# Kernel optimization log

Measured on AMD Instinct MI355X. Metric: run time of the kernel, lower is better.

Reference implementation:

```python
import jax, jax.numpy as jnp
import numpy as np

B, I, O, G = 4096, 256, 256, 8
GRID_MIN, GRID_MAX, RHO = -2.0, 2.0, 1.0


def setup_inputs() -> dict:
    key = jax.random.key(0)
    ks = jax.random.split(key, 8)
    return {
        "x_re": jax.random.normal(ks[0], (B, I), dtype=jnp.float32),
        "x_im": jax.random.normal(ks[1], (B, I), dtype=jnp.float32),
        "realweights": jax.random.normal(ks[2], (I, O, G, G), dtype=jnp.float32),
        "complexweights": jax.random.normal(ks[3], (I, O, G, G), dtype=jnp.float32),
        "silu_weight_re": jax.random.normal(ks[4], (I, O), dtype=jnp.float32),
        "silu_weight_im": jax.random.normal(ks[5], (I, O), dtype=jnp.float32),
        "silu_bias_re": 0.1 * jax.random.normal(ks[6], (I, O), dtype=jnp.float32),
        "silu_bias_im": 0.1 * jax.random.normal(ks[7], (I, O), dtype=jnp.float32),
    }


def reference(x_re, x_im, realweights, complexweights,
              silu_weight_re, silu_weight_im, silu_bias_re, silu_bias_im):
    # Complex grid: grid[u, v] = lin[u] + i * lin[v]
    lin = jnp.linspace(GRID_MIN, GRID_MAX, G, dtype=x_re.dtype)
    # |x - grid|^2 = (x_re - lin_u)^2 + (x_im - lin_v)^2  -> (B, I, G, G)
    dre = x_re[:, :, None, None] - lin[None, None, :, None]
    dim = x_im[:, :, None, None] - lin[None, None, None, :]
    basis = jnp.exp(-(dre * dre + dim * dim) / RHO)  # real-valued (B, I, G, G)
    # RBF contraction: real and imaginary output channels
    out_re = jnp.einsum('biuv,iouv->bo', basis, realweights)
    out_im = jnp.einsum('biuv,iouv->bo', basis, complexweights)
    # Complex SiLU (complex_weight variant): silu applied component-wise,
    # then complex-multiplied by silu_weight, plus bias, summed over i.
    s_re = jax.nn.silu(x_re)  # (B, I)
    s_im = jax.nn.silu(x_im)
    out_re = out_re + s_re @ silu_weight_re - s_im @ silu_weight_im + jnp.sum(silu_bias_re, axis=0)
    out_im = out_im + s_im @ silu_weight_re + s_re @ silu_weight_im + jnp.sum(silu_bias_im, axis=0)
    # Return complex output as stacked (real, imag): (B, O, 2)
    return jnp.stack([out_re, out_im], axis=-1)
```

## Files before the change

kernel.cpp:

```cpp
#include <hip/hip_runtime.h>
#include <hip/hip_fp16.h>
#include <stdint.h>

typedef float floatx4 __attribute__((ext_vector_type(4)));
typedef short short8 __attribute__((ext_vector_type(8)));

constexpr int I_SZ = 256, O_SZ = 256, NCOL = 512, B_SZ = 4096;
constexpr int KSTEPS = 264;
constexpr float GSTEP = 4.0f / 7.0f;
constexpr float NLOG2E = -1.44269504088896f;

__device__ __forceinline__ uint32_t pk_bf16(float lo, float hi) {
  return __builtin_amdgcn_perm(__float_as_uint(hi), __float_as_uint(lo), 0x07060302u);
}
__device__ __forceinline__ short rne_bf16(float f) {
  uint32_t u = __float_as_uint(f);
  return (short)((u + 0x7FFFu + ((u >> 16) & 1u)) >> 16);
}
__device__ __forceinline__ float silu_f(float a) {
  return a * __builtin_amdgcn_rcpf(1.f + __builtin_amdgcn_exp2f(a * NLOG2E));
}
__device__ __forceinline__ void gload_lds16(const void* g, void* l) {
  __builtin_amdgcn_global_load_lds((const __attribute__((address_space(1))) void*)g,
                                   (__attribute__((address_space(3))) void*)l,
                                   16, 0, 0);
}

__global__ void prelude(const float* __restrict__ rw, const float* __restrict__ cw,
                        const float* __restrict__ swre, const float* __restrict__ swim,
                        const float* __restrict__ bre, const float* __restrict__ bim,
                        const float* __restrict__ xre, const float* __restrict__ xim,
                        short* __restrict__ wpack, float* __restrict__ bsum,
                        __half* __restrict__ xT, float* __restrict__ out) {
  __shared__ float tile[64][65];
  const int bid = blockIdx.x, tid = threadIdx.x;

  if (bid < 4224) {
    int idx = bid * 256 + tid;
    int kb = idx >> 12;
    int rem = idx & 4095;
    int n = rem >> 3, gp = rem & 7;
    int g = gp ^ (n & 7);
    int o = n >> 1, c = n & 1;
    float w[8];
    if (kb < 256) {
      const float* W = (c ? cw : rw) + (((size_t)kb * O_SZ + o) << 6) + (g << 3);
      float4 a = *(const float4*)W;
      float4 b = *(const float4*)(W + 4);
      w[0] = a.x; w[1] = a.y; w[2] = a.z; w[3] = a.w;
      w[4] = b.x; w[5] = b.y; w[6] = b.z; w[7] = b.w;
    } else {
      int kp0 = ((kb - 256) << 6) + (g << 3);
      #pragma unroll
      for (int e = 0; e < 8; ++e) {
        int kp = kp0 + e, i = kp >> 1, ci = kp & 1;
        float a = swre[i * O_SZ + o], b = swim[i * O_SZ + o];
        w[e] = (c == 0) ? (ci == 0 ? a : -b) : (ci == 0 ? b : a);
      }
    }
    uint32_t h[8];
    #pragma unroll
    for (int e = 0; e < 8; ++e) h[e] = (uint32_t)(uint16_t)rne_bf16(w[e]);
    uint4 val = make_uint4(h[0] | (h[1] << 16), h[2] | (h[3] << 16),
                           h[4] | (h[5] << 16), h[6] | (h[7] << 16));
    *(uint4*)(wpack + (size_t)idx * 8) = val;
  } else if (bid < 4736) {
    int tb = bid - 4224;
    int bt = tb & 63, it = (tb >> 6) & 3, c = tb >> 8;
    const float* src = (c ? xim : xre);
    int b0 = bt << 6, i0 = it << 6;
    int il = tid & 63, bh = tid >> 6;
    #pragma unroll
    for (int k = 0; k < 16; ++k) {
      int bl = bh + (k << 2);
      tile[bl][il] = src[(size_t)(b0 + bl) * I_SZ + i0 + il];
    }
    __syncthreads();
    int bl2 = tid & 63, ih = tid >> 6;
    __half* dst = xT + ((size_t)c * I_SZ + i0) * B_SZ + b0;
    #pragma unroll
    for (int k = 0; k < 16; ++k) {
      int il2 = ih + (k << 2);
      dst[(size_t)il2 * B_SZ + bl2] = __float2half(tile[bl2][il2]);
    }
  } else if (bid < 4864) {
    int w = tid >> 6, l = tid & 63;
    int n = (bid - 4736) * 4 + w;
    int o = n >> 1;
    const float* src = ((n & 1) ? bim : bre) + o;
    float s = 0.f;
    #pragma unroll
    for (int a = 0; a < 4; ++a) s += src[(size_t)(a * 64 + l) * O_SZ];
    #pragma unroll
    for (int off = 32; off; off >>= 1) s += __shfl_down(s, off, 64);
    if (l == 0) bsum[n] = s;
  } else {
    int z = bid - 4864;
    float4* o4 = (float4*)out;
    float4 zv = {0.f, 0.f, 0.f, 0.f};
    #pragma unroll
    for (int k = 0; k < 4; ++k) o4[(size_t)z * 1024 + k * 256 + tid] = zv;
  }
}

__global__ __launch_bounds__(256, 2) void cvkan_gemm(
    const float* __restrict__ xre, const float* __restrict__ xim,
    const __half* __restrict__ xT,
    const short* __restrict__ wpack, const float* __restrict__ bsum,
    float* __restrict__ out) {
  __shared__ __align__(16) short Bs[2][64 * 64];

  const int tid = threadIdx.x, bid = blockIdx.x;
  const int kch = bid & 7;
  const int rest = bid >> 3;
  const int mt = rest & 15, nt = rest >> 4;
  const int b0 = mt * 256, n0 = nt * 64;
  const int w = tid >> 6, l = tid & 63;
  const int lm = l & 15, q = l >> 4;
  const int row0 = b0 + w * 64 + lm;

  const __half* xTre = xT;
  const __half* xTim = xT + (size_t)I_SZ * B_SZ;

  floatx4 acc[4][4] = {};

  {
    const short* slab = wpack + ((size_t)(kch * 32) * NCOL + n0) * 64 + (w << 10) + (l << 3);
    short* dst = &Bs[0][0] + (w << 10);
    gload_lds16(slab, dst);
    gload_lds16(slab + 512, dst + 512);
  }

  for (int j = 0; j < 33; ++j) {
    const int s = (j < 32) ? (kch * 32 + j) : (256 + kch);

    __syncthreads();

    float xr[4], xi[4];
    if (j < 32) {
      #pragma unroll
      for (int mm = 0; mm < 4; ++mm) {
        const int row = row0 + mm * 16;
        xr[mm] = __half2float(xTre[(size_t)s * B_SZ + row]);
        xi[mm] = __half2float(xTim[(size_t)s * B_SZ + row]);
      }
    }

    if (j < 32) {
      const int s1 = (j < 31) ? (s + 1) : (256 + kch);
      const short* slab = wpack + ((size_t)s1 * NCOL + n0) * 64 + (w << 10) + (l << 3);
      short* dst = &Bs[(j + 1) & 1][0] + (w << 10);
      gload_lds16(slab, dst);
      gload_lds16(slab + 512, dst + 512);
    }

    short8 bf[4][2];
    const short* bp0 = &Bs[j & 1][0];
    #pragma unroll
    for (int nn = 0; nn < 4; ++nn) {
      int c = nn * 16 + lm;
      const short* bp = bp0 + (c << 6);
      bf[nn][0] = *(const short8*)(bp + ((q       ^ (c & 7)) << 3));
      bf[nn][1] = *(const short8*)(bp + (((q + 4) ^ (c & 7)) << 3));
    }

    short8 af[4][2];
    if (j < 32) {
      #pragma unroll
      for (int mm = 0; mm < 4; ++mm) {
        float eiv[8];
        #pragma unroll
        for (int v = 0; v < 8; ++v) {
          float d = xi[mm] - (-2.0f + v * GSTEP);
          eiv[v] = __builtin_amdgcn_exp2f(d * d * NLOG2E);
        }
        float d0 = xr[mm] - (-2.0f + q * GSTEP);
        float d1 = xr[mm] - (-2.0f + (q + 4) * GSTEP);
        float er0 = __builtin_amdgcn_exp2f(d0 * d0 * NLOG2E);
        float er1 = __builtin_amdgcn_exp2f(d1 * d1 * NLOG2E);
        union { short8 v; uint32_t u[4]; } a0, a1;
        #pragma unroll
        for (int t = 0; t < 4; ++t) {
          a0.u[t] = pk_bf16(er0 * eiv[2 * t], er0 * eiv[2 * t + 1]);
          a1.u[t] = pk_bf16(er1 * eiv[2 * t], er1 * eiv[2 * t + 1]);
        }
        af[mm][0] = a0.v;
        af[mm][1] = a1.v;
      }
    } else {
      const int sl = kch;
      #pragma unroll
      for (int mm = 0; mm < 4; ++mm) {
        const int row = row0 + mm * 16;
        #pragma unroll
        for (int kh = 0; kh < 2; ++kh) {
          int i0 = sl * 32 + (q + kh * 4) * 4;
          float4 fr = *(const float4*)(xre + (size_t)row * I_SZ + i0);
          float4 fi = *(const float4*)(xim + (size_t)row * I_SZ + i0);
          union { short8 v; uint32_t u[4]; } a;
          a.u[0] = pk_bf16(silu_f(fr.x), silu_f(fi.x));
          a.u[1] = pk_bf16(silu_f(fr.y), silu_f(fi.y));
          a.u[2] = pk_bf16(silu_f(fr.z), silu_f(fi.z));
          a.u[3] = pk_bf16(silu_f(fr.w), silu_f(fi.w));
          af[mm][kh] = a.v;
        }
      }
    }

    #pragma unroll
    for (int mm = 0; mm < 4; ++mm)
      #pragma unroll
      for (int nn = 0; nn < 4; ++nn) {
        acc[mm][nn] = __builtin_amdgcn_mfma_f32_16x16x32_bf16(af[mm][0], bf[nn][0], acc[mm][nn], 0, 0, 0);
        acc[mm][nn] = __builtin_amdgcn_mfma_f32_16x16x32_bf16(af[mm][1], bf[nn][1], acc[mm][nn], 0, 0, 0);
      }
  }

  #pragma unroll
  for (int nn = 0; nn < 4; ++nn) {
    int col = n0 + nn * 16 + lm;
    float bv = (kch == 7) ? bsum[col] : 0.0f;
    #pragma unroll
    for (int mm = 0; mm < 4; ++mm) {
      int r0 = b0 + w * 64 + mm * 16 + (q << 2);
      #pragma unroll
      for (int r2 = 0; r2 < 4; ++r2)
        atomicAdd(out + (size_t)(r0 + r2) * NCOL + col, acc[mm][nn][r2] + bv);
    }
  }
}

extern "C" void kernel_launch(void* const* d_in, const int* in_sizes, int n_in,
                              void* d_out, int out_size, void* d_ws, size_t ws_size,
                              hipStream_t stream) {
  const float* xre  = (const float*)d_in[0];
  const float* xim  = (const float*)d_in[1];
  const float* rw   = (const float*)d_in[2];
  const float* cw   = (const float*)d_in[3];
  const float* swre = (const float*)d_in[4];
  const float* swim = (const float*)d_in[5];
  const float* bre  = (const float*)d_in[6];
  const float* bim  = (const float*)d_in[7];
  float* out = (float*)d_out;

  size_t wpack_bytes = (size_t)KSTEPS * NCOL * 64 * 2;
  short* wpack = (short*)d_ws;
  float* bsum  = (float*)((char*)d_ws + wpack_bytes);
  __half* xT   = (__half*)((char*)d_ws + wpack_bytes + 4096);

  prelude<<<5376, 256, 0, stream>>>(rw, cw, swre, swim, bre, bim, xre, xim,
                                    wpack, bsum, xT, out);
  cvkan_gemm<<<1024, 256, 0, stream>>>(xre, xim, xT, wpack, bsum, out);
}
```

Baseline: 242.6 us.

## Precompute separable RBF factors in prelude, switch to fp16 MFMA, double M tile

The per-axis Gaussian factors (exp of the real and imaginary distances to each grid line) are now computed once per (i,b) in the prelude and stored as fp16 tables. The GEMM forms the A fragments with packed half multiplies instead of exp2 calls. SiLU values are also precomputed into a table, and weights switch from bf16 to fp16 with f16 MFMA. Each block now covers 512 rows instead of 256 with 8x4 accumulators, which halves the grid and the number of weight reloads. The cost is about 33 MB of extra table traffic, higher register pressure, and fp16 range and precision risk.

```diff
diff --git a/kernel.cpp b/kernel.cpp
--- a/kernel.cpp
+++ b/kernel.cpp
@@ -1,22 +1,15 @@
 #include <hip/hip_runtime.h>
-#include <hip/hip_fp16.h>
 #include <stdint.h>
 
 typedef float floatx4 __attribute__((ext_vector_type(4)));
-typedef short short8 __attribute__((ext_vector_type(8)));
+typedef _Float16 half8 __attribute__((ext_vector_type(8)));
+typedef _Float16 half2t __attribute__((ext_vector_type(2)));
 
 constexpr int I_SZ = 256, O_SZ = 256, NCOL = 512, B_SZ = 4096;
 constexpr int KSTEPS = 264;
 constexpr float GSTEP = 4.0f / 7.0f;
 constexpr float NLOG2E = -1.44269504088896f;
 
-__device__ __forceinline__ uint32_t pk_bf16(float lo, float hi) {
-  return __builtin_amdgcn_perm(__float_as_uint(hi), __float_as_uint(lo), 0x07060302u);
-}
-__device__ __forceinline__ short rne_bf16(float f) {
-  uint32_t u = __float_as_uint(f);
-  return (short)((u + 0x7FFFu + ((u >> 16) & 1u)) >> 16);
-}
 __device__ __forceinline__ float silu_f(float a) {
   return a * __builtin_amdgcn_rcpf(1.f + __builtin_amdgcn_exp2f(a * NLOG2E));
 }
@@ -26,13 +19,17 @@
                                    16, 0, 0);
 }
 
+union H8 { half8 v; half2t h[4]; uint32_t u[4]; };
+
 __global__ void prelude(const float* __restrict__ rw, const float* __restrict__ cw,
                         const float* __restrict__ swre, const float* __restrict__ swim,
                         const float* __restrict__ bre, const float* __restrict__ bim,
                         const float* __restrict__ xre, const float* __restrict__ xim,
-                        short* __restrict__ wpack, float* __restrict__ bsum,
-                        __half* __restrict__ xT, float* __restrict__ out) {
-  __shared__ float tile[64][65];
+                        _Float16* __restrict__ wpack, float* __restrict__ bsum,
+                        _Float16* __restrict__ eivT, _Float16* __restrict__ erqT,
+                        _Float16* __restrict__ sTab, float* __restrict__ out) {
+  __shared__ float tileR[64][65];
+  __shared__ float tileI[64][65];
   const int bid = blockIdx.x, tid = threadIdx.x;
 
   if (bid < 4224) {
@@ -58,34 +55,67 @@
         w[e] = (c == 0) ? (ci == 0 ? a : -b) : (ci == 0 ? b : a);
       }
     }
-    uint32_t h[8];
-    #pragma unroll
-    for (int e = 0; e < 8; ++e) h[e] = (uint32_t)(uint16_t)rne_bf16(w[e]);
-    uint4 val = make_uint4(h[0] | (h[1] << 16), h[2] | (h[3] << 16),
-                           h[4] | (h[5] << 16), h[6] | (h[7] << 16));
-    *(uint4*)(wpack + (size_t)idx * 8) = val;
-  } else if (bid < 4736) {
+    H8 val;
+    #pragma unroll
+    for (int e = 0; e < 8; ++e) val.v[e] = (_Float16)w[e];
+    *(H8*)(wpack + (size_t)idx * 8) = val;
+  } else if (bid < 4480) {
     int tb = bid - 4224;
-    int bt = tb & 63, it = (tb >> 6) & 3, c = tb >> 8;
-    const float* src = (c ? xim : xre);
+    int bt = tb & 63, it = tb >> 6;
     int b0 = bt << 6, i0 = it << 6;
     int il = tid & 63, bh = tid >> 6;
     #pragma unroll
     for (int k = 0; k < 16; ++k) {
       int bl = bh + (k << 2);
-      tile[bl][il] = src[(size_t)(b0 + bl) * I_SZ + i0 + il];
+      tileR[bl][il] = xre[(size_t)(b0 + bl) * I_SZ + i0 + il];
+      tileI[bl][il] = xim[(size_t)(b0 + bl) * I_SZ + i0 + il];
     }
     __syncthreads();
-    int bl2 = tid & 63, ih = tid >> 6;
-    __half* dst = xT + ((size_t)c * I_SZ + i0) * B_SZ + b0;
     #pragma unroll
     for (int k = 0; k < 16; ++k) {
-      int il2 = ih + (k << 2);
-      dst[(size_t)il2 * B_SZ + bl2] = __float2half(tile[bl2][il2]);
-    }
-  } else if (bid < 4864) {
+      int p = k * 256 + tid;
+      int i_l = p >> 6, b_l = p & 63;
+      float xr = tileR[b_l][i_l];
+      float xi = tileI[b_l][i_l];
+      float eru[8], eiv[8];
+      #pragma unroll
+      for (int g = 0; g < 8; ++g) {
+        float dr = xr - (-2.0f + g * GSTEP);
+        float di = xi - (-2.0f + g * GSTEP);
+        eru[g] = __builtin_amdgcn_exp2f(dr * dr * NLOG2E);
+        eiv[g] = __builtin_amdgcn_exp2f(di * di * NLOG2E);
+      }
+      size_t base = ((size_t)(i0 + i_l) * B_SZ + b0 + b_l) * 8;
+      H8 ev, eq;
+      #pragma unroll
+      for (int g = 0; g < 8; ++g) ev.v[g] = (_Float16)eiv[g];
+      #pragma unroll
+      for (int q = 0; q < 4; ++q) { eq.v[2 * q] = (_Float16)eru[q]; eq.v[2 * q + 1] = (_Float16)eru[q + 4]; }
+      *(H8*)(eivT + base) = ev;
+      *(H8*)(erqT + base) = eq;
+    }
+  } else if (bid < 4992) {
+    int tg = (bid - 4480) * 256 + tid;
+    int b = tg >> 5, io = (tg & 31) << 3;
+    const float* pr = xre + (size_t)b * I_SZ + io;
+    const float* pi = xim + (size_t)b * I_SZ + io;
+    float4 r0 = *(const float4*)pr, r1 = *(const float4*)(pr + 4);
+    float4 q0 = *(const float4*)pi, q1 = *(const float4*)(pi + 4);
+    H8 lo, hi;
+    lo.v[0] = (_Float16)silu_f(r0.x); lo.v[1] = (_Float16)silu_f(q0.x);
+    lo.v[2] = (_Float16)silu_f(r0.y); lo.v[3] = (_Float16)silu_f(q0.y);
+    lo.v[4] = (_Float16)silu_f(r0.z); lo.v[5] = (_Float16)silu_f(q0.z);
+    lo.v[6] = (_Float16)silu_f(r0.w); lo.v[7] = (_Float16)silu_f(q0.w);
+    hi.v[0] = (_Float16)silu_f(r1.x); hi.v[1] = (_Float16)silu_f(q1.x);
+    hi.v[2] = (_Float16)silu_f(r1.y); hi.v[3] = (_Float16)silu_f(q1.y);
+    hi.v[4] = (_Float16)silu_f(r1.z); hi.v[5] = (_Float16)silu_f(q1.z);
+    hi.v[6] = (_Float16)silu_f(r1.w); hi.v[7] = (_Float16)silu_f(q1.w);
+    _Float16* dst = sTab + (size_t)b * 512 + 2 * io;
+    *(H8*)dst = lo;
+    *(H8*)(dst + 8) = hi;
+  } else if (bid < 5120) {
     int w = tid >> 6, l = tid & 63;
-    int n = (bid - 4736) * 4 + w;
+    int n = (bid - 4992) * 4 + w;
     int o = n >> 1;
     const float* src = ((n & 1) ? bim : bre) + o;
     float s = 0.f;
@@ -95,7 +125,7 @@
     for (int off = 32; off; off >>= 1) s += __shfl_down(s, off, 64);
     if (l == 0) bsum[n] = s;
   } else {
-    int z = bid - 4864;
+    int z = bid - 5120;
     float4* o4 = (float4*)out;
     float4 zv = {0.f, 0.f, 0.f, 0.f};
     #pragma unroll
@@ -104,29 +134,26 @@
 }
 
 __global__ __launch_bounds__(256, 2) void cvkan_gemm(
-    const float* __restrict__ xre, const float* __restrict__ xim,
-    const __half* __restrict__ xT,
-    const short* __restrict__ wpack, const float* __restrict__ bsum,
+    const _Float16* __restrict__ eivT, const _Float16* __restrict__ erqT,
+    const _Float16* __restrict__ sTab,
+    const _Float16* __restrict__ wpack, const float* __restrict__ bsum,
     float* __restrict__ out) {
-  __shared__ __align__(16) short Bs[2][64 * 64];
+  __shared__ __align__(16) _Float16 Bs[2][64 * 64];
 
   const int tid = threadIdx.x, bid = blockIdx.x;
   const int kch = bid & 7;
   const int rest = bid >> 3;
-  const int mt = rest & 15, nt = rest >> 4;
-  const int b0 = mt * 256, n0 = nt * 64;
+  const int mt = rest & 7, nt = rest >> 3;
+  const int b0 = mt * 512, n0 = nt * 64;
   const int w = tid >> 6, l = tid & 63;
   const int lm = l & 15, q = l >> 4;
-  const int row0 = b0 + w * 64 + lm;
-
-  const __half* xTre = xT;
-  const __half* xTim = xT + (size_t)I_SZ * B_SZ;
-
-  floatx4 acc[4][4] = {};
+  const int row0 = b0 + w * 128 + lm;
+
+  floatx4 acc[8][4] = {};
 
   {
-    const short* slab = wpack + ((size_t)(kch * 32) * NCOL + n0) * 64 + (w << 10) + (l << 3);
-    short* dst = &Bs[0][0] + (w << 10);
+    const _Float16* slab = wpack + ((size_t)(kch * 32) * NCOL + n0) * 64 + (w << 10) + (l << 3);
+    _Float16* dst = &Bs[0][0] + (w << 10);
     gload_lds16(slab, dst);
     gload_lds16(slab + 512, dst + 512);
   }
@@ -136,84 +163,62 @@
 
     __syncthreads();
 
-    float xr[4], xi[4];
+    half8 eivr[8]; half2t erqr[8];
+    half8 afs[8][2];
     if (j < 32) {
       #pragma unroll
-      for (int mm = 0; mm < 4; ++mm) {
-        const int row = row0 + mm * 16;
-        xr[mm] = __half2float(xTre[(size_t)s * B_SZ + row]);
-        xi[mm] = __half2float(xTim[(size_t)s * B_SZ + row]);
+      for (int mm = 0; mm < 8; ++mm) {
+        size_t base = ((size_t)s * B_SZ + row0 + mm * 16) * 8;
+        eivr[mm] = *(const half8*)(eivT + base);
+        erqr[mm] = *(const half2t*)(erqT + base + (q << 1));
+      }
+    } else {
+      #pragma unroll
+      for (int mm = 0; mm < 8; ++mm) {
+        const _Float16* p = sTab + (size_t)(row0 + mm * 16) * 512 + kch * 64 + (q << 3);
+        afs[mm][0] = *(const half8*)p;
+        afs[mm][1] = *(const half8*)(p + 32);
       }
     }
 
     if (j < 32) {
       const int s1 = (j < 31) ? (s + 1) : (256 + kch);
-      const short* slab = wpack + ((size_t)s1 * NCOL + n0) * 64 + (w << 10) + (l << 3);
-      short* dst = &Bs[(j + 1) & 1][0] + (w << 10);
+      const _Float16* slab = wpack + ((size_t)s1 * NCOL + n0) * 64 + (w << 10) + (l << 3);
+      _Float16* dst = &Bs[(j + 1) & 1][0] + (w << 10);
       gload_lds16(slab, dst);
       gload_lds16(slab + 512, dst + 512);
     }
 
-    short8 bf[4][2];
-    const short* bp0 = &Bs[j & 1][0];
+    half8 bf[4][2];
+    const _Float16* bp0 = &Bs[j & 1][0];
     #pragma unroll
     for (int nn = 0; nn < 4; ++nn) {
       int c = nn * 16 + lm;
-      const short* bp = bp0 + (c << 6);
-      bf[nn][0] = *(const short8*)(bp + ((q       ^ (c & 7)) << 3));
-      bf[nn][1] = *(const short8*)(bp + (((q + 4) ^ (c & 7)) << 3));
-    }
-
-    short8 af[4][2];
-    if (j < 32) {
-      #pragma unroll
-      for (int mm = 0; mm < 4; ++mm) {
-        float eiv[8];
+      const _Float16* bp = bp0 + (c << 6);
+      bf[nn][0] = *(const half8*)(bp + ((q       ^ (c & 7)) << 3));
+      bf[nn][1] = *(const half8*)(bp + (((q + 4) ^ (c & 7)) << 3));
+    }
+
+    #pragma unroll
+    for (int mm = 0; mm < 8; ++mm) {
+      half8 a0, a1;
+      if (j < 32) {
+        H8 ev; ev.v = eivr[mm];
+        half2t e0 = {erqr[mm].x, erqr[mm].x};
+        half2t e1 = {erqr[mm].y, erqr[mm].y};
+        H8 r0, r1;
         #pragma unroll
-        for (int v = 0; v < 8; ++v) {
-          float d = xi[mm] - (-2.0f + v * GSTEP);
-          eiv[v] = __builtin_amdgcn_exp2f(d * d * NLOG2E);
-        }
-        float d0 = xr[mm] - (-2.0f + q * GSTEP);
-        float d1 = xr[mm] - (-2.0f + (q + 4) * GSTEP);
-        float er0 = __builtin_amdgcn_exp2f(d0 * d0 * NLOG2E);
-        float er1 = __builtin_amdgcn_exp2f(d1 * d1 * NLOG2E);
-        union { short8 v; uint32_t u[4]; } a0, a1;
-        #pragma unroll
-        for (int t = 0; t < 4; ++t) {
-          a0.u[t] = pk_bf16(er0 * eiv[2 * t], er0 * eiv[2 * t + 1]);
-          a1.u[t] = pk_bf16(er1 * eiv[2 * t], er1 * eiv[2 * t + 1]);
-        }
-        af[mm][0] = a0.v;
-        af[mm][1] = a1.v;
-      }
-    } else {
-      const int sl = kch;
-      #pragma unroll
-      for (int mm = 0; mm < 4; ++mm) {
-        const int row = row0 + mm * 16;
-        #pragma unroll
-        for (int kh = 0; kh < 2; ++kh) {
-          int i0 = sl * 32 + (q + kh * 4) * 4;
-          float4 fr = *(const float4*)(xre + (size_t)row * I_SZ + i0);
-          float4 fi = *(const float4*)(xim + (size_t)row * I_SZ + i0);
-          union { short8 v; uint32_t u[4]; } a;
-          a.u[0] = pk_bf16(silu_f(fr.x), silu_f(fi.x));
-          a.u[1] = pk_bf16(silu_f(fr.y), silu_f(fi.y));
-          a.u[2] = pk_bf16(silu_f(fr.z), silu_f(fi.z));
-          a.u[3] = pk_bf16(silu_f(fr.w), silu_f(fi.w));
-          af[mm][kh] = a.v;
-        }
-      }
-    }
-
-    #pragma unroll
-    for (int mm = 0; mm < 4; ++mm)
+        for (int t = 0; t < 4; ++t) { r0.h[t] = e0 * ev.h[t]; r1.h[t] = e1 * ev.h[t]; }
+        a0 = r0.v; a1 = r1.v;
+      } else {
+        a0 = afs[mm][0]; a1 = afs[mm][1];
+      }
       #pragma unroll
       for (int nn = 0; nn < 4; ++nn) {
-        acc[mm][nn] = __builtin_amdgcn_mfma_f32_16x16x32_bf16(af[mm][0], bf[nn][0], acc[mm][nn], 0, 0, 0);
-        acc[mm][nn] = __builtin_amdgcn_mfma_f32_16x16x32_bf16(af[mm][1], bf[nn][1], acc[mm][nn], 0, 0, 0);
-      }
+        acc[mm][nn] = __builtin_amdgcn_mfma_f32_16x16x32_f16(a0, bf[nn][0], acc[mm][nn], 0, 0, 0);
+        acc[mm][nn] = __builtin_amdgcn_mfma_f32_16x16x32_f16(a1, bf[nn][1], acc[mm][nn], 0, 0, 0);
+      }
+    }
   }
 
   #pragma unroll
@@ -221,8 +226,8 @@
     int col = n0 + nn * 16 + lm;
     float bv = (kch == 7) ? bsum[col] : 0.0f;
     #pragma unroll
-    for (int mm = 0; mm < 4; ++mm) {
-      int r0 = b0 + w * 64 + mm * 16 + (q << 2);
+    for (int mm = 0; mm < 8; ++mm) {
+      int r0 = b0 + w * 128 + mm * 16 + (q << 2);
       #pragma unroll
       for (int r2 = 0; r2 < 4; ++r2)
         atomicAdd(out + (size_t)(r0 + r2) * NCOL + col, acc[mm][nn][r2] + bv);
@@ -243,12 +248,14 @@
   const float* bim  = (const float*)d_in[7];
   float* out = (float*)d_out;
 
-  size_t wpack_bytes = (size_t)KSTEPS * NCOL * 64 * 2;
-  short* wpack = (short*)d_ws;
-  float* bsum  = (float*)((char*)d_ws + wpack_bytes);
-  __half* xT   = (__half*)((char*)d_ws + wpack_bytes + 4096);
-
-  prelude<<<5376, 256, 0, stream>>>(rw, cw, swre, swim, bre, bim, xre, xim,
-                                    wpack, bsum, xT, out);
-  cvkan_gemm<<<1024, 256, 0, stream>>>(xre, xim, xT, wpack, bsum, out);
-}
+  size_t off = 0;
+  _Float16* wpack = (_Float16*)((char*)d_ws + off); off += (size_t)KSTEPS * NCOL * 64 * 2;
+  _Float16* eivT  = (_Float16*)((char*)d_ws + off); off += (size_t)I_SZ * B_SZ * 8 * 2;
+  _Float16* erqT  = (_Float16*)((char*)d_ws + off); off += (size_t)I_SZ * B_SZ * 8 * 2;
+  _Float16* sTab  = (_Float16*)((char*)d_ws + off); off += (size_t)B_SZ * 512 * 2;
+  float*    bsum  = (float*)((char*)d_ws + off);
+
+  prelude<<<5632, 256, 0, stream>>>(rw, cw, swre, swim, bre, bim, xre, xim,
+                                    wpack, bsum, eivT, erqT, sTab, out);
+  cvkan_gemm<<<512, 256, 0, stream>>>(eivT, erqT, sTab, wpack, bsum, out);
+}
```

Measured after the change: 233.0 us. 1.04x faster.
